# Kernel tuning notes

Hardware: AMD Instinct MI355X
Metric: run time of the kernel (lower is better)

The kernel has to match this reference:

```python
import jax, jax.numpy as jnp
import numpy as np

N, E, D, DE = 40000, 640000, 128, 64
LAMDA = 0.5
NEG_SLOPE = 0.01  # F.leaky_relu default


def setup_inputs() -> dict:
    key = jax.random.key(0)
    ks = jax.random.split(key, 8)
    node_h = jax.random.normal(ks[0], (N, D), dtype=jnp.float32)
    edge_h = jax.random.normal(ks[1], (E, DE), dtype=jnp.float32)
    src = jax.random.randint(ks[2], (E,), 0, N)
    dst = jax.random.randint(ks[3], (E,), 0, N)
    # parameters (torch Linear layout: [out, in])
    fc_w = jax.random.normal(ks[4], (D, D), dtype=jnp.float32) / np.sqrt(D)
    edge_fc_w = jax.random.normal(ks[5], (DE, DE), dtype=jnp.float32) / np.sqrt(DE)
    edge_fc_b = jax.random.normal(ks[6], (DE,), dtype=jnp.float32) * 0.01
    attn_w = jax.random.normal(ks[7], (1, 2 * D + DE), dtype=jnp.float32) / np.sqrt(2 * D + DE)
    return {"node_h": node_h, "edge_h": edge_h, "src": src, "dst": dst,
            "fc_w": fc_w, "edge_fc_w": edge_fc_w, "edge_fc_b": edge_fc_b, "attn_w": attn_w}


def reference(node_h, edge_h, src, dst, fc_w, edge_fc_w, edge_fc_b, attn_w):
    n = node_h.shape[0]
    z = node_h @ fc_w.T                       # [N, D]
    edge_z = edge_h @ edge_fc_w.T + edge_fc_b  # [E, DE]
    # attn_fc(concat([z_src, z_dst, edge_z])) == z_src@w_s + z_dst@w_d + edge_z@w_e
    w = attn_w[0]
    w_s, w_d, w_e = w[:D], w[D:2 * D], w[2 * D:]
    s_node = z @ w_s                           # [N]
    d_node = z @ w_d                           # [N]
    e = s_node[src] + d_node[dst] + edge_z @ w_e  # [E]
    e = jax.nn.leaky_relu(e, NEG_SLOPE)
    # segment softmax over incoming edges of each dst node
    m = jax.ops.segment_max(e, dst, num_segments=n)          # [N]
    ex = jnp.exp(e - m[dst])                                  # [E]
    denom = jax.ops.segment_sum(ex, dst, num_segments=n)     # [N]
    alpha = ex / denom[dst]                                   # [E]
    h = jax.ops.segment_sum(alpha[:, None] * z[src], dst, num_segments=n)  # [N, D]
    return (1.0 - LAMDA) * node_h + LAMDA * h
```

## Files before the change

kernel.cpp:

```cpp
#include <hip/hip_runtime.h>

#define NNODE 40000
#define NEDGE 640000
#define DD 128
#define DE 64
#define SLOT 64

typedef float fvec4 __attribute__((ext_vector_type(4)));

__device__ __forceinline__ unsigned short f2bf(float f) {
    union { float f; unsigned int i; } c; c.f = f;
    unsigned int b = c.i;
    return (unsigned short)((b + 0x7fffu + ((b >> 16) & 1u)) >> 16);
}

__global__ __launch_bounds__(128) void node_z(
        const float* __restrict__ node_h,
        const float* __restrict__ fc_w,
        const float* __restrict__ attw,
        const float* __restrict__ efw,
        const float* __restrict__ efb,
        unsigned int* __restrict__ z_bf,
        float* __restrict__ s_node,
        float* __restrict__ d_node,
        float* __restrict__ vc,
        int* __restrict__ deg) {
    int t = threadIdx.x;

    int zi = blockIdx.x * 128 + t;
    if (zi < NNODE) deg[zi] = 0;

    if (blockIdx.x == 0) {
        if (t < DE) {
            float acc = 0.f;
            for (int j = 0; j < DE; ++j)
                acc += efw[j * DE + t] * attw[2 * DD + j];
            vc[t] = acc;
        }
        if (t == 0) {
            float acc = 0.f;
            for (int j = 0; j < DE; ++j)
                acc += efb[j] * attw[2 * DD + j];
            vc[DE] = acc;
        }
    }

    float4 wreg[DD / 4];
    const float4* wr = (const float4*)(fc_w + t * DD);
#pragma unroll
    for (int i = 0; i < DD / 4; ++i) wreg[i] = wr[i];
    float ws_att = attw[t];
    float wd_att = attw[DD + t];

    __shared__ float x0[DD], x1[DD];
    __shared__ float red[4][2];

    for (int nb = blockIdx.x * 2; nb < NNODE; nb += gridDim.x * 2) {
        __syncthreads();
        x0[t] = node_h[(size_t)nb * DD + t];
        x1[t] = node_h[(size_t)(nb + 1) * DD + t];
        __syncthreads();
        const float4* xv0 = (const float4*)x0;
        const float4* xv1 = (const float4*)x1;
        float acc0 = 0.f, acc1 = 0.f;
#pragma unroll
        for (int i = 0; i < DD / 4; ++i) {
            float4 a = wreg[i];
            float4 b0 = xv0[i];
            float4 b1 = xv1[i];
            acc0 += a.x * b0.x + a.y * b0.y + a.z * b0.z + a.w * b0.w;
            acc1 += a.x * b1.x + a.y * b1.y + a.z * b1.z + a.w * b1.w;
        }
        float nxt0 = __shfl_down(acc0, 1, 64);
        float nxt1 = __shfl_down(acc1, 1, 64);
        if ((t & 1) == 0) {
            unsigned int p0 = (unsigned int)f2bf(acc0) |
                              ((unsigned int)f2bf(nxt0) << 16);
            unsigned int p1 = (unsigned int)f2bf(acc1) |
                              ((unsigned int)f2bf(nxt1) << 16);
            z_bf[(size_t)nb * (DD / 2) + (t >> 1)]       = p0;
            z_bf[(size_t)(nb + 1) * (DD / 2) + (t >> 1)] = p1;
        }

        float s0 = acc0 * ws_att, d0 = acc0 * wd_att;
        float s1 = acc1 * ws_att, d1 = acc1 * wd_att;
#pragma unroll
        for (int off = 32; off > 0; off >>= 1) {
            s0 += __shfl_down(s0, off, 64);
            d0 += __shfl_down(d0, off, 64);
            s1 += __shfl_down(s1, off, 64);
            d1 += __shfl_down(d1, off, 64);
        }
        int wv = t >> 6;
        if ((t & 63) == 0) {
            red[0][wv] = s0; red[1][wv] = d0;
            red[2][wv] = s1; red[3][wv] = d1;
        }
        __syncthreads();
        if (t == 0) {
            s_node[nb]     = red[0][0] + red[0][1];
            d_node[nb]     = red[1][0] + red[1][1];
            s_node[nb + 1] = red[2][0] + red[2][1];
            d_node[nb + 1] = red[3][0] + red[3][1];
        }
    }
}

__global__ __launch_bounds__(256) void edge_all(
        const float* __restrict__ edge_h,
        const float* __restrict__ vc,
        const int* __restrict__ src,
        const int* __restrict__ dst,
        const float* __restrict__ s_node,
        const float* __restrict__ d_node,
        int* __restrict__ deg,
        int2* __restrict__ se_s) {
    __shared__ float v[DE + 1];
    int t = threadIdx.x;
    if (t <= DE) v[t] = vc[t];
    __syncthreads();

    int lane = t & 63;
    int wave = t >> 6;
    int sub  = lane & 3;
    int eslot = lane >> 2;
    int e0 = blockIdx.x * 128 + wave * 32 + eslot;
    int e1 = e0 + 16;

    const fvec4* eh0 = (const fvec4*)(edge_h + (size_t)e0 * DE) + sub * 4;
    const fvec4* eh1 = (const fvec4*)(edge_h + (size_t)e1 * DE) + sub * 4;
    fvec4 a0 = eh0[0], a1 = eh0[1], a2 = eh0[2], a3 = eh0[3];
    fvec4 b0 = eh1[0], b1 = eh1[1], b2 = eh1[2], b3 = eh1[3];

    bool fin = (sub & 1) == 0;
    int fe = (sub == 0) ? e0 : e1;
    int fs = 0, fd = 0;
    float fsn = 0.f, fdn = 0.f;
    if (fin) {
        fs = src[fe];
        fd = dst[fe];
        fsn = s_node[fs];
        fdn = d_node[fd];
    }

    const float* vv = &v[16 * sub];
    float d0 = a0.x * vv[0]  + a0.y * vv[1]  + a0.z * vv[2]  + a0.w * vv[3]
             + a1.x * vv[4]  + a1.y * vv[5]  + a1.z * vv[6]  + a1.w * vv[7]
             + a2.x * vv[8]  + a2.y * vv[9]  + a2.z * vv[10] + a2.w * vv[11]
             + a3.x * vv[12] + a3.y * vv[13] + a3.z * vv[14] + a3.w * vv[15];
    float d1 = b0.x * vv[0]  + b0.y * vv[1]  + b0.z * vv[2]  + b0.w * vv[3]
             + b1.x * vv[4]  + b1.y * vv[5]  + b1.z * vv[6]  + b1.w * vv[7]
             + b2.x * vv[8]  + b2.y * vv[9]  + b2.z * vv[10] + b2.w * vv[11]
             + b3.x * vv[12] + b3.y * vv[13] + b3.z * vv[14] + b3.w * vv[15];
    d0 += __shfl_xor(d0, 1, 64);
    d0 += __shfl_xor(d0, 2, 64);
    d1 += __shfl_xor(d1, 1, 64);
    d1 += __shfl_xor(d1, 2, 64);

    if (fin) {
        float ev = fsn + fdn + ((sub == 0) ? d0 : d1) + v[DE];
        ev = ev > 0.f ? ev : 0.01f * ev;
        float ex = __expf(ev);
        int r = atomicAdd(&deg[fd], 1);
        if (r < SLOT) se_s[fd * SLOT + r] = make_int2(fs, __float_as_int(ex));
    }
}

__device__ __forceinline__ void acc8(float* a, uint4 w, float ex) {
    a[0] += ex * __uint_as_float(w.x << 16);
    a[1] += ex * __uint_as_float(w.x & 0xffff0000u);
    a[2] += ex * __uint_as_float(w.y << 16);
    a[3] += ex * __uint_as_float(w.y & 0xffff0000u);
    a[4] += ex * __uint_as_float(w.z << 16);
    a[5] += ex * __uint_as_float(w.z & 0xffff0000u);
    a[6] += ex * __uint_as_float(w.w << 16);
    a[7] += ex * __uint_as_float(w.w & 0xffff0000u);
}

__global__ __launch_bounds__(256) void gather_kernel(
        const float* __restrict__ node_h,
        const uint4* __restrict__ z_bf,
        const int* __restrict__ deg,
        const int2* __restrict__ se_s,
        float* __restrict__ out) {
    int wave = threadIdx.x >> 6;
    int lane = threadIdx.x & 63;
    int quarter = lane >> 4;
    int hl = lane & 15;
    int n = blockIdx.x * 4 + wave;

    size_t o = (size_t)n * (DD / 4) + 2 * hl;
    fvec4 nh0 = {0.f, 0.f, 0.f, 0.f}, nh1 = {0.f, 0.f, 0.f, 0.f};
    if (quarter == 0) {
        nh0 = ((const fvec4*)node_h)[o];
        nh1 = ((const fvec4*)node_h)[o + 1];
    }

    int beg = n * SLOT;
    int dc = deg[n];
    dc = dc < SLOT ? dc : SLOT;
    int end = beg + dc;

    float a[8] = {0.f, 0.f, 0.f, 0.f, 0.f, 0.f, 0.f, 0.f};
    float den = 0.f;
    int j = beg + quarter;
    for (; j + 12 < end; j += 16) {
        int2 se0 = se_s[j];
        int2 se1 = se_s[j + 4];
        int2 se2 = se_s[j + 8];
        int2 se3 = se_s[j + 12];
        uint4 w0 = z_bf[(size_t)se0.x * 16 + hl];
        uint4 w1 = z_bf[(size_t)se1.x * 16 + hl];
        uint4 w2 = z_bf[(size_t)se2.x * 16 + hl];
        uint4 w3 = z_bf[(size_t)se3.x * 16 + hl];
        float ex0 = __int_as_float(se0.y);
        float ex1 = __int_as_float(se1.y);
        float ex2 = __int_as_float(se2.y);
        float ex3 = __int_as_float(se3.y);
        acc8(a, w0, ex0);
        acc8(a, w1, ex1);
        acc8(a, w2, ex2);
        acc8(a, w3, ex3);
        den += (ex0 + ex1) + (ex2 + ex3);
    }
    for (; j + 4 < end; j += 8) {
        int2 se0 = se_s[j];
        int2 se1 = se_s[j + 4];
        uint4 w0 = z_bf[(size_t)se0.x * 16 + hl];
        uint4 w1 = z_bf[(size_t)se1.x * 16 + hl];
        float ex0 = __int_as_float(se0.y);
        float ex1 = __int_as_float(se1.y);
        acc8(a, w0, ex0);
        acc8(a, w1, ex1);
        den += ex0 + ex1;
    }
    if (j < end) {
        int2 se = se_s[j];
        uint4 w = z_bf[(size_t)se.x * 16 + hl];
        float ex = __int_as_float(se.y);
        acc8(a, w, ex);
        den += ex;
    }

#pragma unroll
    for (int k = 0; k < 8; ++k) {
        a[k] += __shfl_xor(a[k], 16, 64);
        a[k] += __shfl_xor(a[k], 32, 64);
    }
    den += __shfl_xor(den, 16, 64);
    den += __shfl_xor(den, 32, 64);

    if (quarter == 0) {
        float inv = den > 0.f ? 0.5f / den : 0.f;
        fvec4 r0, r1;
        r0.x = 0.5f * nh0.x + a[0] * inv;
        r0.y = 0.5f * nh0.y + a[1] * inv;
        r0.z = 0.5f * nh0.z + a[2] * inv;
        r0.w = 0.5f * nh0.w + a[3] * inv;
        r1.x = 0.5f * nh1.x + a[4] * inv;
        r1.y = 0.5f * nh1.y + a[5] * inv;
        r1.z = 0.5f * nh1.z + a[6] * inv;
        r1.w = 0.5f * nh1.w + a[7] * inv;
        __builtin_nontemporal_store(r0, (fvec4*)out + o);
        __builtin_nontemporal_store(r1, (fvec4*)out + o + 1);
    }
}

extern "C" void kernel_launch(void* const* d_in, const int* in_sizes, int n_in,
                              void* d_out, int out_size, void* d_ws, size_t ws_size,
                              hipStream_t stream) {
    const float* node_h    = (const float*)d_in[0];
    const float* edge_h    = (const float*)d_in[1];
    const int*   src       = (const int*)d_in[2];
    const int*   dst       = (const int*)d_in[3];
    const float* fc_w      = (const float*)d_in[4];
    const float* edge_fc_w = (const float*)d_in[5];
    const float* edge_fc_b = (const float*)d_in[6];
    const float* attn_w    = (const float*)d_in[7];
    float* out = (float*)d_out;

    char* ws = (char*)d_ws;
    unsigned int* z_bf = (unsigned int*)ws;
    int2*  se_s   = (int2*)(ws + (size_t)NNODE * 64 * 4);
    float* s_node = (float*)(se_s + (size_t)NNODE * SLOT);
    float* d_node = s_node + NNODE;
    float* vc     = d_node + NNODE;
    int*   deg    = (int*)(vc + 128);

    node_z<<<2048, 128, 0, stream>>>(node_h, fc_w, attn_w, edge_fc_w,
                                     edge_fc_b, z_bf, s_node, d_node, vc, deg);
    edge_all<<<NEDGE / 128, 256, 0, stream>>>(edge_h, vc, src, dst,
                                              s_node, d_node, deg, se_s);
    gather_kernel<<<NNODE / 4, 256, 0, stream>>>(node_h, (const uint4*)z_bf,
                                                 deg, se_s, out);
}
```

Measured before the change: 363.5 us.

## Fold attention weights into fc_w, split s/d node scores, coalesce edge loads

Precomputes us = fc_w^T w_s and ud = fc_w^T w_d once, and computes s_node/d_node in a new sdnode kernel straight from node_h. This removes the per-node cross-wave reductions and extra syncs from node_z, which now handles four nodes per iteration. edge_all now loads edge_h fully coalesced into a skewed LDS buffer before the per-edge dot product. The cost is an extra kernel launch and an extra read of node_h, plus more LDS use in edge_all.

```diff
diff --git a/kernel.cpp b/kernel.cpp
--- a/kernel.cpp
+++ b/kernel.cpp
@@ -21,9 +21,9 @@
         const float* __restrict__ efw,
         const float* __restrict__ efb,
         unsigned int* __restrict__ z_bf,
-        float* __restrict__ s_node,
-        float* __restrict__ d_node,
         float* __restrict__ vc,
+        float* __restrict__ us,
+        float* __restrict__ ud,
         int* __restrict__ deg) {
     int t = threadIdx.x;
 
@@ -31,6 +31,14 @@
     if (zi < NNODE) deg[zi] = 0;
 
     if (blockIdx.x == 0) {
+        float as = 0.f, ad = 0.f;
+        for (int i = 0; i < DD; ++i) {
+            float w = fc_w[i * DD + t];
+            as += w * attw[i];
+            ad += w * attw[DD + i];
+        }
+        us[t] = as;
+        ud[t] = ad;
         if (t < DE) {
             float acc = 0.f;
             for (int j = 0; j < DE; ++j)
@@ -49,61 +57,96 @@
     const float4* wr = (const float4*)(fc_w + t * DD);
 #pragma unroll
     for (int i = 0; i < DD / 4; ++i) wreg[i] = wr[i];
-    float ws_att = attw[t];
-    float wd_att = attw[DD + t];
-
-    __shared__ float x0[DD], x1[DD];
-    __shared__ float red[4][2];
-
-    for (int nb = blockIdx.x * 2; nb < NNODE; nb += gridDim.x * 2) {
+
+    __shared__ float x[4][DD];
+
+    for (int nb = blockIdx.x * 4; nb < NNODE; nb += gridDim.x * 4) {
         __syncthreads();
-        x0[t] = node_h[(size_t)nb * DD + t];
-        x1[t] = node_h[(size_t)(nb + 1) * DD + t];
+#pragma unroll
+        for (int ni = 0; ni < 4; ++ni)
+            x[ni][t] = node_h[(size_t)(nb + ni) * DD + t];
         __syncthreads();
-        const float4* xv0 = (const float4*)x0;
-        const float4* xv1 = (const float4*)x1;
-        float acc0 = 0.f, acc1 = 0.f;
+        const float4* xv0 = (const float4*)x[0];
+        const float4* xv1 = (const float4*)x[1];
+        const float4* xv2 = (const float4*)x[2];
+        const float4* xv3 = (const float4*)x[3];
+        float a0 = 0.f, a1 = 0.f, a2 = 0.f, a3 = 0.f;
 #pragma unroll
         for (int i = 0; i < DD / 4; ++i) {
-            float4 a = wreg[i];
-            float4 b0 = xv0[i];
-            float4 b1 = xv1[i];
-            acc0 += a.x * b0.x + a.y * b0.y + a.z * b0.z + a.w * b0.w;
-            acc1 += a.x * b1.x + a.y * b1.y + a.z * b1.z + a.w * b1.w;
-        }
-        float nxt0 = __shfl_down(acc0, 1, 64);
-        float nxt1 = __shfl_down(acc1, 1, 64);
+            float4 w = wreg[i];
+            float4 b0 = xv0[i], b1 = xv1[i], b2 = xv2[i], b3 = xv3[i];
+            a0 += w.x * b0.x + w.y * b0.y + w.z * b0.z + w.w * b0.w;
+            a1 += w.x * b1.x + w.y * b1.y + w.z * b1.z + w.w * b1.w;
+            a2 += w.x * b2.x + w.y * b2.y + w.z * b2.z + w.w * b2.w;
+            a3 += w.x * b3.x + w.y * b3.y + w.z * b3.z + w.w * b3.w;
+        }
+        float n0 = __shfl_down(a0, 1, 64);
+        float n1 = __shfl_down(a1, 1, 64);
+        float n2 = __shfl_down(a2, 1, 64);
+        float n3 = __shfl_down(a3, 1, 64);
         if ((t & 1) == 0) {
-            unsigned int p0 = (unsigned int)f2bf(acc0) |
-                              ((unsigned int)f2bf(nxt0) << 16);
-            unsigned int p1 = (unsigned int)f2bf(acc1) |
-                              ((unsigned int)f2bf(nxt1) << 16);
-            z_bf[(size_t)nb * (DD / 2) + (t >> 1)]       = p0;
-            z_bf[(size_t)(nb + 1) * (DD / 2) + (t >> 1)] = p1;
-        }
-
-        float s0 = acc0 * ws_att, d0 = acc0 * wd_att;
-        float s1 = acc1 * ws_att, d1 = acc1 * wd_att;
-#pragma unroll
-        for (int off = 32; off > 0; off >>= 1) {
-            s0 += __shfl_down(s0, off, 64);
-            d0 += __shfl_down(d0, off, 64);
-            s1 += __shfl_down(s1, off, 64);
-            d1 += __shfl_down(d1, off, 64);
-        }
-        int wv = t >> 6;
-        if ((t & 63) == 0) {
-            red[0][wv] = s0; red[1][wv] = d0;
-            red[2][wv] = s1; red[3][wv] = d1;
-        }
-        __syncthreads();
-        if (t == 0) {
-            s_node[nb]     = red[0][0] + red[0][1];
-            d_node[nb]     = red[1][0] + red[1][1];
-            s_node[nb + 1] = red[2][0] + red[2][1];
-            d_node[nb + 1] = red[3][0] + red[3][1];
-        }
-    }
+            int c = t >> 1;
+            z_bf[(size_t)(nb + 0) * (DD / 2) + c] =
+                (unsigned int)f2bf(a0) | ((unsigned int)f2bf(n0) << 16);
+            z_bf[(size_t)(nb + 1) * (DD / 2) + c] =
+                (unsigned int)f2bf(a1) | ((unsigned int)f2bf(n1) << 16);
+            z_bf[(size_t)(nb + 2) * (DD / 2) + c] =
+                (unsigned int)f2bf(a2) | ((unsigned int)f2bf(n2) << 16);
+            z_bf[(size_t)(nb + 3) * (DD / 2) + c] =
+                (unsigned int)f2bf(a3) | ((unsigned int)f2bf(n3) << 16);
+        }
+    }
+}
+
+__global__ __launch_bounds__(256) void sdnode(
+        const float* __restrict__ node_h,
+        const float* __restrict__ us,
+        const float* __restrict__ ud,
+        float* __restrict__ s_node,
+        float* __restrict__ d_node) {
+    __shared__ float xbuf[4][16 * DD];
+    __shared__ float u2[2][DD];
+    int t = threadIdx.x;
+    if (t < DD) u2[0][t] = us[t];
+    else        u2[1][t - DD] = ud[t - DD];
+
+    int lane = t & 63;
+    int wave = t >> 6;
+    int nbase = blockIdx.x * 64 + wave * 16;
+
+    const fvec4* gp = (const fvec4*)(node_h + (size_t)nbase * DD);
+    fvec4 st[8];
+#pragma unroll
+    for (int i = 0; i < 8; ++i) st[i] = gp[i * 64 + lane];
+
+    fvec4* lp = (fvec4*)xbuf[wave];
+#pragma unroll
+    for (int i = 0; i < 8; ++i) {
+        int e = i * 2 + (lane >> 5);
+        int j = lane & 31;
+        lp[e * 32 + ((j + e) & 31)] = st[i];
+    }
+    __syncthreads();
+
+    int nloc = lane >> 2;
+    int q = lane & 3;
+    float ps = 0.f, pd = 0.f;
+#pragma unroll
+    for (int jj = 0; jj < 8; ++jj) {
+        int j = q * 8 + jj;
+        fvec4 x = lp[nloc * 32 + ((j + nloc) & 31)];
+        const float* a = &u2[0][j * 4];
+        const float* b = &u2[1][j * 4];
+        ps += x.x * a[0] + x.y * a[1] + x.z * a[2] + x.w * a[3];
+        pd += x.x * b[0] + x.y * b[1] + x.z * b[2] + x.w * b[3];
+    }
+    ps += __shfl_xor(ps, 1, 64);
+    ps += __shfl_xor(ps, 2, 64);
+    pd += __shfl_xor(pd, 1, 64);
+    pd += __shfl_xor(pd, 2, 64);
+    int n = nbase + nloc;
+    if (q == 0) s_node[n] = ps;
+    if (q == 1) d_node[n] = pd;
 }
 
 __global__ __launch_bounds__(256) void edge_all(
@@ -116,49 +159,52 @@
         int* __restrict__ deg,
         int2* __restrict__ se_s) {
     __shared__ float v[DE + 1];
+    __shared__ float ebuf[4][32 * DE];
     int t = threadIdx.x;
     if (t <= DE) v[t] = vc[t];
-    __syncthreads();
 
     int lane = t & 63;
     int wave = t >> 6;
-    int sub  = lane & 3;
-    int eslot = lane >> 2;
-    int e0 = blockIdx.x * 128 + wave * 32 + eslot;
-    int e1 = e0 + 16;
-
-    const fvec4* eh0 = (const fvec4*)(edge_h + (size_t)e0 * DE) + sub * 4;
-    const fvec4* eh1 = (const fvec4*)(edge_h + (size_t)e1 * DE) + sub * 4;
-    fvec4 a0 = eh0[0], a1 = eh0[1], a2 = eh0[2], a3 = eh0[3];
-    fvec4 b0 = eh1[0], b1 = eh1[1], b2 = eh1[2], b3 = eh1[3];
-
-    bool fin = (sub & 1) == 0;
-    int fe = (sub == 0) ? e0 : e1;
+    int ebase = blockIdx.x * 128 + wave * 32;
+
+    const fvec4* gp = (const fvec4*)(edge_h + (size_t)ebase * DE);
+    fvec4 st[8];
+#pragma unroll
+    for (int i = 0; i < 8; ++i) st[i] = gp[i * 64 + lane];
+
+    int h = lane & 1;
+    int eloc = lane >> 1;
+    int ge = ebase + eloc;
     int fs = 0, fd = 0;
     float fsn = 0.f, fdn = 0.f;
-    if (fin) {
-        fs = src[fe];
-        fd = dst[fe];
+    if (h == 0) {
+        fs = src[ge];
+        fd = dst[ge];
         fsn = s_node[fs];
         fdn = d_node[fd];
     }
 
-    const float* vv = &v[16 * sub];
-    float d0 = a0.x * vv[0]  + a0.y * vv[1]  + a0.z * vv[2]  + a0.w * vv[3]
-             + a1.x * vv[4]  + a1.y * vv[5]  + a1.z * vv[6]  + a1.w * vv[7]
-             + a2.x * vv[8]  + a2.y * vv[9]  + a2.z * vv[10] + a2.w * vv[11]
-             + a3.x * vv[12] + a3.y * vv[13] + a3.z * vv[14] + a3.w * vv[15];
-    float d1 = b0.x * vv[0]  + b0.y * vv[1]  + b0.z * vv[2]  + b0.w * vv[3]
-             + b1.x * vv[4]  + b1.y * vv[5]  + b1.z * vv[6]  + b1.w * vv[7]
-             + b2.x * vv[8]  + b2.y * vv[9]  + b2.z * vv[10] + b2.w * vv[11]
-             + b3.x * vv[12] + b3.y * vv[13] + b3.z * vv[14] + b3.w * vv[15];
-    d0 += __shfl_xor(d0, 1, 64);
-    d0 += __shfl_xor(d0, 2, 64);
-    d1 += __shfl_xor(d1, 1, 64);
-    d1 += __shfl_xor(d1, 2, 64);
-
-    if (fin) {
-        float ev = fsn + fdn + ((sub == 0) ? d0 : d1) + v[DE];
+    fvec4* lp = (fvec4*)ebuf[wave];
+#pragma unroll
+    for (int i = 0; i < 8; ++i) {
+        int e = i * 4 + (lane >> 4);
+        int j = lane & 15;
+        lp[e * 16 + ((j + e) & 15)] = st[i];
+    }
+    __syncthreads();
+
+    float d = 0.f;
+#pragma unroll
+    for (int jj = 0; jj < 8; ++jj) {
+        int j = h * 8 + jj;
+        fvec4 x = lp[eloc * 16 + ((j + eloc) & 15)];
+        const float* vv = &v[j * 4];
+        d += x.x * vv[0] + x.y * vv[1] + x.z * vv[2] + x.w * vv[3];
+    }
+    d += __shfl_xor(d, 1, 64);
+
+    if (h == 0) {
+        float ev = fsn + fdn + d + v[DE];
         ev = ev > 0.f ? ev : 0.01f * ev;
         float ex = __expf(ev);
         int r = atomicAdd(&deg[fd], 1);
@@ -286,9 +332,12 @@
     float* d_node = s_node + NNODE;
     float* vc     = d_node + NNODE;
     int*   deg    = (int*)(vc + 128);
+    float* us     = (float*)(deg + NNODE);
+    float* ud     = us + 128;
 
     node_z<<<2048, 128, 0, stream>>>(node_h, fc_w, attn_w, edge_fc_w,
-                                     edge_fc_b, z_bf, s_node, d_node, vc, deg);
+                                     edge_fc_b, z_bf, vc, us, ud, deg);
+    sdnode<<<NNODE / 64, 256, 0, stream>>>(node_h, us, ud, s_node, d_node);
     edge_all<<<NEDGE / 128, 256, 0, stream>>>(edge_h, vc, src, dst,
                                               s_node, d_node, deg, se_s);
     gather_kernel<<<NNODE / 4, 256, 0, stream>>>(node_h, (const uint4*)z_bf,
```

Measured after the change: 345.1 us. 5.1% less time.
